# Optimization experiments

Measured on AMD Instinct MI355X. Metric: run time of the kernel, lower is better.

Reference implementation:

```python
import jax, jax.numpy as jnp
import numpy as np

B, N = 256, 256


def greedy_hard_perm(soft_perm):
    # soft_perm: (B, N, N). Sequential greedy masked-argmax assignment, vectorized over batch.
    Bn, Nn, _ = soft_perm.shape
    NEG = jnp.finfo(soft_perm.dtype).min
    b_idx = jnp.arange(Bn)

    def step(carry, _):
        scores, hard, row_mask, col_mask = carry
        # mask out already-assigned rows/cols (in-place masked_fill_ in torch -> carried scores)
        scores = jnp.where(row_mask[:, :, None], NEG, scores)
        scores = jnp.where(col_mask[:, None, :], NEG, scores)
        flat_idx = jnp.argmax(scores.reshape(Bn, -1), axis=1)  # (B,)
        r = flat_idx // Nn
        c = flat_idx % Nn
        hard = hard.at[b_idx, r, c].set(1.0)
        row_mask = row_mask.at[b_idx, r].set(True)
        col_mask = col_mask.at[b_idx, c].set(True)
        return (scores, hard, row_mask, col_mask), None

    init = (
        soft_perm,
        jnp.zeros_like(soft_perm),
        jnp.zeros((Bn, Nn), dtype=bool),
        jnp.zeros((Bn, Nn), dtype=bool),
    )
    (_, hard, _, _), _ = jax.lax.scan(step, init, None, length=Nn)
    return hard


def setup_inputs() -> dict:
    key = jax.random.key(0)
    logits = jax.random.normal(key, (B, N, N), dtype=jnp.float32)
    # realistic soft permutation: row-stochastic scores
    soft_perm = jax.nn.softmax(logits, axis=-1)
    return {"soft_perm": soft_perm}


def reference(soft_perm):
    # hard perm carries no gradient (built from constant 1.0 writes in torch)
    hard = greedy_hard_perm(jax.lax.stop_gradient(soft_perm))
    # straight-through estimator: forward = hard, backward = identity through soft
    return hard + soft_perm - jax.lax.stop_gradient(soft_perm)
```

## Files before the change

### kernel.cpp

```cpp
#include <hip/hip_runtime.h>
#include <math.h>

#define NEGINF (-INFINITY)
#define NEGINF_BITS ((int)0xFF800000)

typedef unsigned int u32;
typedef unsigned long long u64;

#define RST 64

__device__ __forceinline__ int rl_i(int x, int l) {
    return __builtin_amdgcn_readlane(x, l);
}
__device__ __forceinline__ float rl_f(float x, int l) {
    return __int_as_float(__builtin_amdgcn_readlane(__float_as_int(x), l));
}

template <int CTRL>
__device__ __forceinline__ float dppmax(float x) {
    int xi = __float_as_int(x);
    int yi = __builtin_amdgcn_update_dpp(xi, xi, CTRL, 0xf, 0xf, false);
    return fmaxf(x, __int_as_float(yi));
}

__device__ __forceinline__ float wave_max64(float x) {
    x = dppmax<0x111>(x);
    x = dppmax<0x112>(x);
    x = dppmax<0x114>(x);
    x = dppmax<0x118>(x);
    x = dppmax<0x142>(x);
    x = dppmax<0x143>(x);
    return rl_f(x, 63);
}

__device__ __forceinline__ void wave_argmax(float v, int idx, float& out_v, int& out_idx) {
    float mv = wave_max64(v);
    u64 mask = __ballot(v == mv);
    int ln = (int)__builtin_ctzll(mask);
    int bi = rl_i(idx, ln);
    u64 rest = mask & (mask - 1);
    if (rest) {
        while (rest) {
            int l2 = (int)__builtin_ctzll(rest); rest &= rest - 1;
            int b2 = rl_i(idx, l2);
            if (b2 < bi) bi = b2;
        }
    }
    out_v = mv; out_idx = bi;
}

__device__ __forceinline__ void wave_top2(float lv, int lf, float lv2, int lf2,
                                          float& nv, int& nc, float& nv2, int& nc2) {
    float av = lv, bv = lv2;
#define T2STAGE(CTRL) {                                                        \
        float a2 = __int_as_float(__builtin_amdgcn_update_dpp(                 \
            NEGINF_BITS, __float_as_int(av), CTRL, 0xf, 0xf, false));          \
        float b2 = __int_as_float(__builtin_amdgcn_update_dpp(                 \
            NEGINF_BITS, __float_as_int(bv), CTRL, 0xf, 0xf, false));          \
        float t = fminf(av, a2);                                               \
        av = fmaxf(av, a2);                                                    \
        bv = fmaxf(fmaxf(bv, b2), t); }
    T2STAGE(0x111) T2STAGE(0x112) T2STAGE(0x114) T2STAGE(0x118)
    T2STAGE(0x142) T2STAGE(0x143)
#undef T2STAGE
    nv = rl_f(av, 63);
    float sv = rl_f(bv, 63);

    u64 m1 = __ballot(lv == nv);
    int ln = (int)__builtin_ctzll(m1);
    nc = rl_i(lf, ln);

    nv2 = sv; nc2 = 300;
    if (sv > 0.f) {
        if (sv == nv) {
            float b2v = rl_f(lv2, ln);
            if (b2v == nv) {
                nc2 = rl_i(lf2, ln);
            } else {
                u64 rest = m1 & (m1 - 1);
                int l2 = (int)__builtin_ctzll(rest);
                nc2 = rl_i(lf, l2);
            }
        } else {
            u64 m2 = __ballot(lv == sv || lv2 == sv);
            int l2 = (int)__builtin_ctzll(m2);
            float tl = rl_f(lv, l2);
            nc2 = (tl == sv) ? rl_i(lf, l2) : rl_i(lf2, l2);
        }
    }
}

__global__ __launch_bounds__(64, 1) void greedy_perm_kernel(
        const float* __restrict__ soft, float* __restrict__ out) {
    __shared__ float smem[RST * 256];
    const int b = blockIdx.x;
    const int lane = threadIdx.x;
    const size_t base = (size_t)b << 16;
    const float* sc = soft + base;
    float* ob = out + base;

    float rv[4], spv[4];
    int   rc[4], spc[4];
#pragma unroll
    for (int j = 0; j < 4; ++j) { rv[j] = NEGINF; rc[j] = 0; spv[j] = NEGINF; spc[j] = 300; }

    const float4 zero4 = make_float4(0.f, 0.f, 0.f, 0.f);

    for (int k = 0; k < 64; k += 4) {
        float4 w[4][4];
#pragma unroll
        for (int j = 0; j < 4; ++j) {
            const float4* rp = (const float4*)(sc + (size_t)(j * 64 + lane) * 256);
#pragma unroll
            for (int kk = 0; kk < 4; ++kk) w[j][kk] = rp[k + kk];
        }
#pragma unroll
        for (int j = 0; j < 4; ++j) {
            float4* op = (float4*)(ob + (size_t)(j * 64 + lane) * 256);
#pragma unroll
            for (int kk = 0; kk < 4; ++kk) op[k + kk] = zero4;
        }
        {
            float* lp = &smem[lane << 8];
#pragma unroll
            for (int kk = 0; kk < 4; ++kk)
                *(float4*)&lp[((k + kk) ^ lane) << 2] = w[0][kk];
        }
#pragma unroll
        for (int j = 0; j < 4; ++j) {
#pragma unroll
            for (int kk = 0; kk < 4; ++kk) {
                const float4 ww = w[j][kk];
                const int bc = 4 * (k + kk);
                const float e[4] = {ww.x, ww.y, ww.z, ww.w};
#pragma unroll
                for (int q = 0; q < 4; ++q) {
                    const float x = e[q];
                    const int   cx = bc + q;
                    const bool g1 = x > rv[j];
                    const bool g2 = x > spv[j];
                    spv[j] = g1 ? rv[j] : (g2 ? x  : spv[j]);
                    spc[j] = g1 ? rc[j] : (g2 ? cx : spc[j]);
                    rv[j]  = g1 ? x  : rv[j];
                    rc[j]  = g1 ? cx : rc[j];
                }
            }
        }
    }

    __threadfence_block();

    u32 colmask = 0;

    for (int step = 0; step < 256; ++step) {
        float bv = rv[0];
        int   bf = (lane << 8) | (rc[0] & 255);
#pragma unroll
        for (int j = 1; j < 4; ++j) {
            if (rv[j] > bv) { bv = rv[j]; bf = (((j << 6) + lane) << 8) | (rc[j] & 255); }
        }
        float gv; int gf;
        wave_argmax(bv, bf, gv, gf);
        (void)gv;
        const int r  = gf >> 8;
        const int cc = gf & 255;

        if (lane == 0) ob[gf] = 1.0f;
        if (lane == (r & 63)) {
            const int rj = r >> 6;
#pragma unroll
            for (int j = 0; j < 4; ++j) if (j == rj) { rv[j] = NEGINF; rc[j] = 300; }
        }
        if (lane == (cc >> 2)) colmask |= 1u << (cc & 3);

#pragma unroll
        for (int j = 0; j < 4; ++j) if (spc[j] == cc) spc[j] = 300;

        bool dd[4]; bool anyd = false;
#pragma unroll
        for (int j = 0; j < 4; ++j) { dd[j] = (rc[j] == cc); anyd |= dd[j]; }
        if (__ballot(anyd)) {
#pragma unroll
            for (int j = 0; j < 4; ++j) {
                const bool need = dd[j] && (spc[j] == 300);
                if (dd[j] && !need) {
                    rv[j] = spv[j]; rc[j] = spc[j];
                    spv[j] = NEGINF; spc[j] = 300;
                }
                u64 m = __ballot(need);
                while (m) {
                    const int ln = (int)__builtin_ctzll(m); m &= m - 1;
                    const int row = (j << 6) + ln;
                    float4 w = (row < RST)
                        ? *(const float4*)&smem[(row << 8) | (((lane ^ ln) & 63) << 2)]
                        : *(const float4*)(sc + ((size_t)row << 8) + (lane << 2));
                    const float q0 = (colmask & 1u) ? NEGINF : w.x;
                    const float q1 = (colmask & 2u) ? NEGINF : w.y;
                    const float q2 = (colmask & 4u) ? NEGINF : w.z;
                    const float q3 = (colmask & 8u) ? NEGINF : w.w;
                    const int cb = lane << 2;
                    float lv = q0; int lf = cb;
                    float lv2 = NEGINF; int lf2 = cb;
                    {
                        bool g1 = q1 > lv, g2 = q1 > lv2;
                        lv2 = g1 ? lv : (g2 ? q1 : lv2); lf2 = g1 ? lf : (g2 ? cb + 1 : lf2);
                        lv  = g1 ? q1 : lv;              lf  = g1 ? cb + 1 : lf;
                        g1 = q2 > lv; g2 = q2 > lv2;
                        lv2 = g1 ? lv : (g2 ? q2 : lv2); lf2 = g1 ? lf : (g2 ? cb + 2 : lf2);
                        lv  = g1 ? q2 : lv;              lf  = g1 ? cb + 2 : lf;
                        g1 = q3 > lv; g2 = q3 > lv2;
                        lv2 = g1 ? lv : (g2 ? q3 : lv2); lf2 = g1 ? lf : (g2 ? cb + 3 : lf2);
                        lv  = g1 ? q3 : lv;              lf  = g1 ? cb + 3 : lf;
                    }
                    float nv, nv2; int nc, nc2;
                    wave_top2(lv, lf, lv2, lf2, nv, nc, nv2, nc2);
                    if (lane == ln) {
#pragma unroll
                        for (int jj = 0; jj < 4; ++jj) if (jj == j) {
                            rv[jj] = nv; rc[jj] = nc;
                            spv[jj] = nv2; spc[jj] = nc2;
                        }
                    }
                }
            }
        }
    }
}

extern "C" void kernel_launch(void* const* d_in, const int* in_sizes, int n_in,
                              void* d_out, int out_size, void* d_ws, size_t ws_size,
                              hipStream_t stream) {
    const float* soft = (const float*)d_in[0];
    float* out = (float*)d_out;
    const int n_batches = in_sizes[0] >> 16;

    greedy_perm_kernel<<<n_batches, 64, 0, stream>>>(soft, out);
}
```

Before: 300.9 us.

## Process two batches per wavefront with interleaved dual argmax reductions

Each 64-lane block now handles two batch matrices, interleaving their sequential greedy steps so the DPP max reductions, ballots and readlanes of the two independent chains can overlap and hide latency. The grid is halved to 128 blocks on a GPU with 256 CUs, so half the compute units sit idle. Shared-memory row caching per batch drops from 64 to 32 rows, so more refills must fall back to global loads. Register pressure roughly doubles.

```diff
diff --git a/kernel.cpp b/kernel.cpp
--- a/kernel.cpp
+++ b/kernel.cpp
@@ -7,7 +7,7 @@
 typedef unsigned int u32;
 typedef unsigned long long u64;
 
-#define RST 64
+#define RSTB 32
 
 __device__ __forceinline__ int rl_i(int x, int l) {
     return __builtin_amdgcn_readlane(x, l);
@@ -23,30 +23,50 @@
     return fmaxf(x, __int_as_float(yi));
 }
 
+template <int CTRL>
+__device__ __forceinline__ void dppmax2(float& a, float& b) {
+    int ai = __float_as_int(a), bi = __float_as_int(b);
+    int a2 = __builtin_amdgcn_update_dpp(ai, ai, CTRL, 0xf, 0xf, false);
+    int b2 = __builtin_amdgcn_update_dpp(bi, bi, CTRL, 0xf, 0xf, false);
+    a = fmaxf(a, __int_as_float(a2));
+    b = fmaxf(b, __int_as_float(b2));
+}
+
 __device__ __forceinline__ float wave_max64(float x) {
-    x = dppmax<0x111>(x);
-    x = dppmax<0x112>(x);
-    x = dppmax<0x114>(x);
-    x = dppmax<0x118>(x);
-    x = dppmax<0x142>(x);
-    x = dppmax<0x143>(x);
+    x = dppmax<0x111>(x); x = dppmax<0x112>(x); x = dppmax<0x114>(x);
+    x = dppmax<0x118>(x); x = dppmax<0x142>(x); x = dppmax<0x143>(x);
     return rl_f(x, 63);
 }
 
-__device__ __forceinline__ void wave_argmax(float v, int idx, float& out_v, int& out_idx) {
-    float mv = wave_max64(v);
-    u64 mask = __ballot(v == mv);
-    int ln = (int)__builtin_ctzll(mask);
-    int bi = rl_i(idx, ln);
-    u64 rest = mask & (mask - 1);
-    if (rest) {
-        while (rest) {
-            int l2 = (int)__builtin_ctzll(rest); rest &= rest - 1;
-            int b2 = rl_i(idx, l2);
-            if (b2 < bi) bi = b2;
-        }
-    }
-    out_v = mv; out_idx = bi;
+__device__ __forceinline__ void wave_argmax_dual(float vA, int idxA, float vB, int idxB,
+                                                 int& gfA, int& gfB) {
+    float xA = vA, xB = vB;
+    dppmax2<0x111>(xA, xB); dppmax2<0x112>(xA, xB); dppmax2<0x114>(xA, xB);
+    dppmax2<0x118>(xA, xB); dppmax2<0x142>(xA, xB); dppmax2<0x143>(xA, xB);
+    const float mvA = rl_f(xA, 63);
+    const float mvB = rl_f(xB, 63);
+    u64 mA = __ballot(vA == mvA);
+    u64 mB = __ballot(vB == mvB);
+    int lnA = (int)__builtin_ctzll(mA);
+    int lnB = (int)__builtin_ctzll(mB);
+    gfA = rl_i(idxA, lnA);
+    gfB = rl_i(idxB, lnB);
+    u64 rA = mA & (mA - 1);
+    u64 rB = mB & (mB - 1);
+    if (rA) {
+        while (rA) {
+            int l2 = (int)__builtin_ctzll(rA); rA &= rA - 1;
+            int f2 = rl_i(idxA, l2);
+            if (f2 < gfA) gfA = f2;
+        }
+    }
+    if (rB) {
+        while (rB) {
+            int l2 = (int)__builtin_ctzll(rB); rB &= rB - 1;
+            int f2 = rl_i(idxB, l2);
+            if (f2 < gfB) gfB = f2;
+        }
+    }
 }
 
 __device__ __forceinline__ void wave_top2(float lv, int lf, float lv2, int lf2,
@@ -91,58 +111,81 @@
 }
 
 __global__ __launch_bounds__(64, 1) void greedy_perm_kernel(
-        const float* __restrict__ soft, float* __restrict__ out) {
-    __shared__ float smem[RST * 256];
-    const int b = blockIdx.x;
+        const float* __restrict__ soft, float* __restrict__ out, int ntot) {
+    __shared__ float smem[2 * RSTB * 256];
     const int lane = threadIdx.x;
-    const size_t base = (size_t)b << 16;
-    const float* sc = soft + base;
-    float* ob = out + base;
-
-    float rv[4], spv[4];
-    int   rc[4], spc[4];
-#pragma unroll
-    for (int j = 0; j < 4; ++j) { rv[j] = NEGINF; rc[j] = 0; spv[j] = NEGINF; spc[j] = 300; }
+    const int b0 = blockIdx.x * 2;
+    const int b1 = (b0 + 1 < ntot) ? (b0 + 1) : b0;
+    const float* scA = soft + ((size_t)b0 << 16);
+    const float* scB = soft + ((size_t)b1 << 16);
+    float* obA = out + ((size_t)b0 << 16);
+    float* obB = out + ((size_t)b1 << 16);
+    float* smA = smem;
+    float* smB = smem + RSTB * 256;
+
+    float rvA[4], s1vA[4], rvB[4], s1vB[4];
+    int   rcA[4], s1cA[4], rcB[4], s1cB[4];
+#pragma unroll
+    for (int j = 0; j < 4; ++j) {
+        rvA[j] = NEGINF; rcA[j] = 0; s1vA[j] = NEGINF; s1cA[j] = 300;
+        rvB[j] = NEGINF; rcB[j] = 0; s1vB[j] = NEGINF; s1cB[j] = 300;
+    }
 
     const float4 zero4 = make_float4(0.f, 0.f, 0.f, 0.f);
 
     for (int k = 0; k < 64; k += 4) {
-        float4 w[4][4];
+        float4 wA[4][4], wB[4][4];
 #pragma unroll
         for (int j = 0; j < 4; ++j) {
-            const float4* rp = (const float4*)(sc + (size_t)(j * 64 + lane) * 256);
-#pragma unroll
-            for (int kk = 0; kk < 4; ++kk) w[j][kk] = rp[k + kk];
+            const float4* rpA = (const float4*)(scA + (size_t)(j * 64 + lane) * 256);
+            const float4* rpB = (const float4*)(scB + (size_t)(j * 64 + lane) * 256);
+#pragma unroll
+            for (int kk = 0; kk < 4; ++kk) { wA[j][kk] = rpA[k + kk]; wB[j][kk] = rpB[k + kk]; }
         }
 #pragma unroll
         for (int j = 0; j < 4; ++j) {
-            float4* op = (float4*)(ob + (size_t)(j * 64 + lane) * 256);
-#pragma unroll
-            for (int kk = 0; kk < 4; ++kk) op[k + kk] = zero4;
-        }
-        {
-            float* lp = &smem[lane << 8];
-#pragma unroll
-            for (int kk = 0; kk < 4; ++kk)
-                *(float4*)&lp[((k + kk) ^ lane) << 2] = w[0][kk];
+            float4* opA = (float4*)(obA + (size_t)(j * 64 + lane) * 256);
+            float4* opB = (float4*)(obB + (size_t)(j * 64 + lane) * 256);
+#pragma unroll
+            for (int kk = 0; kk < 4; ++kk) { opA[k + kk] = zero4; opB[k + kk] = zero4; }
+        }
+        if (lane < RSTB) {
+            float* lpA = &smA[lane << 8];
+            float* lpB = &smB[lane << 8];
+#pragma unroll
+            for (int kk = 0; kk < 4; ++kk) {
+                *(float4*)&lpA[((k + kk) ^ lane) << 2] = wA[0][kk];
+                *(float4*)&lpB[((k + kk) ^ lane) << 2] = wB[0][kk];
+            }
         }
 #pragma unroll
         for (int j = 0; j < 4; ++j) {
 #pragma unroll
             for (int kk = 0; kk < 4; ++kk) {
-                const float4 ww = w[j][kk];
                 const int bc = 4 * (k + kk);
-                const float e[4] = {ww.x, ww.y, ww.z, ww.w};
+                const float eA[4] = {wA[j][kk].x, wA[j][kk].y, wA[j][kk].z, wA[j][kk].w};
+                const float eB[4] = {wB[j][kk].x, wB[j][kk].y, wB[j][kk].z, wB[j][kk].w};
 #pragma unroll
                 for (int q = 0; q < 4; ++q) {
-                    const float x = e[q];
-                    const int   cx = bc + q;
-                    const bool g1 = x > rv[j];
-                    const bool g2 = x > spv[j];
-                    spv[j] = g1 ? rv[j] : (g2 ? x  : spv[j]);
-                    spc[j] = g1 ? rc[j] : (g2 ? cx : spc[j]);
-                    rv[j]  = g1 ? x  : rv[j];
-                    rc[j]  = g1 ? cx : rc[j];
+                    const int cx = bc + q;
+                    {
+                        const float x = eA[q];
+                        const bool g1 = x > rvA[j];
+                        const bool g2 = x > s1vA[j];
+                        s1vA[j] = g1 ? rvA[j] : (g2 ? x  : s1vA[j]);
+                        s1cA[j] = g1 ? rcA[j] : (g2 ? cx : s1cA[j]);
+                        rvA[j]  = g1 ? x  : rvA[j];
+                        rcA[j]  = g1 ? cx : rcA[j];
+                    }
+                    {
+                        const float x = eB[q];
+                        const bool g1 = x > rvB[j];
+                        const bool g2 = x > s1vB[j];
+                        s1vB[j] = g1 ? rvB[j] : (g2 ? x  : s1vB[j]);
+                        s1cB[j] = g1 ? rcB[j] : (g2 ? cx : s1cB[j]);
+                        rvB[j]  = g1 ? x  : rvB[j];
+                        rcB[j]  = g1 ? cx : rcB[j];
+                    }
                 }
             }
         }
@@ -150,54 +193,67 @@
 
     __threadfence_block();
 
-    u32 colmask = 0;
+    u32 cmA = 0, cmB = 0;
 
     for (int step = 0; step < 256; ++step) {
-        float bv = rv[0];
-        int   bf = (lane << 8) | (rc[0] & 255);
+        float bvA = rvA[0]; int bfA = (lane << 8) | (rcA[0] & 255);
+        float bvB = rvB[0]; int bfB = (lane << 8) | (rcB[0] & 255);
 #pragma unroll
         for (int j = 1; j < 4; ++j) {
-            if (rv[j] > bv) { bv = rv[j]; bf = (((j << 6) + lane) << 8) | (rc[j] & 255); }
-        }
-        float gv; int gf;
-        wave_argmax(bv, bf, gv, gf);
-        (void)gv;
-        const int r  = gf >> 8;
-        const int cc = gf & 255;
-
-        if (lane == 0) ob[gf] = 1.0f;
-        if (lane == (r & 63)) {
-            const int rj = r >> 6;
-#pragma unroll
-            for (int j = 0; j < 4; ++j) if (j == rj) { rv[j] = NEGINF; rc[j] = 300; }
-        }
-        if (lane == (cc >> 2)) colmask |= 1u << (cc & 3);
-
-#pragma unroll
-        for (int j = 0; j < 4; ++j) if (spc[j] == cc) spc[j] = 300;
-
-        bool dd[4]; bool anyd = false;
-#pragma unroll
-        for (int j = 0; j < 4; ++j) { dd[j] = (rc[j] == cc); anyd |= dd[j]; }
-        if (__ballot(anyd)) {
+            if (rvA[j] > bvA) { bvA = rvA[j]; bfA = (((j << 6) + lane) << 8) | (rcA[j] & 255); }
+            if (rvB[j] > bvB) { bvB = rvB[j]; bfB = (((j << 6) + lane) << 8) | (rcB[j] & 255); }
+        }
+
+        int gfA, gfB;
+        wave_argmax_dual(bvA, bfA, bvB, bfB, gfA, gfB);
+        const int rA = gfA >> 8, ccA = gfA & 255;
+        const int rB = gfB >> 8, ccB = gfB & 255;
+
+        if (lane == 0) { obA[gfA] = 1.0f; obB[gfB] = 1.0f; }
+
+        if (lane == (rA & 63)) {
+            const int rj = rA >> 6;
+#pragma unroll
+            for (int j = 0; j < 4; ++j) if (j == rj) { rvA[j] = NEGINF; rcA[j] = 300; }
+        }
+        if (lane == (ccA >> 2)) cmA |= 1u << (ccA & 3);
+#pragma unroll
+        for (int j = 0; j < 4; ++j) if (s1cA[j] == ccA) s1cA[j] = 300;
+        bool ddA[4]; bool anydA = false;
+#pragma unroll
+        for (int j = 0; j < 4; ++j) { ddA[j] = (rcA[j] == ccA); anydA |= ddA[j]; }
+
+        if (lane == (rB & 63)) {
+            const int rj = rB >> 6;
+#pragma unroll
+            for (int j = 0; j < 4; ++j) if (j == rj) { rvB[j] = NEGINF; rcB[j] = 300; }
+        }
+        if (lane == (ccB >> 2)) cmB |= 1u << (ccB & 3);
+#pragma unroll
+        for (int j = 0; j < 4; ++j) if (s1cB[j] == ccB) s1cB[j] = 300;
+        bool ddB[4]; bool anydB = false;
+#pragma unroll
+        for (int j = 0; j < 4; ++j) { ddB[j] = (rcB[j] == ccB); anydB |= ddB[j]; }
+
+        if (__ballot(anydA)) {
 #pragma unroll
             for (int j = 0; j < 4; ++j) {
-                const bool need = dd[j] && (spc[j] == 300);
-                if (dd[j] && !need) {
-                    rv[j] = spv[j]; rc[j] = spc[j];
-                    spv[j] = NEGINF; spc[j] = 300;
+                const bool need = ddA[j] && (s1cA[j] == 300);
+                if (ddA[j] && !need) {
+                    rvA[j] = s1vA[j]; rcA[j] = s1cA[j];
+                    s1vA[j] = NEGINF; s1cA[j] = 300;
                 }
                 u64 m = __ballot(need);
                 while (m) {
                     const int ln = (int)__builtin_ctzll(m); m &= m - 1;
                     const int row = (j << 6) + ln;
-                    float4 w = (row < RST)
-                        ? *(const float4*)&smem[(row << 8) | (((lane ^ ln) & 63) << 2)]
-                        : *(const float4*)(sc + ((size_t)row << 8) + (lane << 2));
-                    const float q0 = (colmask & 1u) ? NEGINF : w.x;
-                    const float q1 = (colmask & 2u) ? NEGINF : w.y;
-                    const float q2 = (colmask & 4u) ? NEGINF : w.z;
-                    const float q3 = (colmask & 8u) ? NEGINF : w.w;
+                    float4 w = (row < RSTB)
+                        ? *(const float4*)&smA[(row << 8) | (((lane ^ ln) & 63) << 2)]
+                        : *(const float4*)(scA + ((size_t)row << 8) + (lane << 2));
+                    const float q0 = (cmA & 1u) ? NEGINF : w.x;
+                    const float q1 = (cmA & 2u) ? NEGINF : w.y;
+                    const float q2 = (cmA & 4u) ? NEGINF : w.z;
+                    const float q3 = (cmA & 8u) ? NEGINF : w.w;
                     const int cb = lane << 2;
                     float lv = q0; int lf = cb;
                     float lv2 = NEGINF; int lf2 = cb;
@@ -217,8 +273,54 @@
                     if (lane == ln) {
 #pragma unroll
                         for (int jj = 0; jj < 4; ++jj) if (jj == j) {
-                            rv[jj] = nv; rc[jj] = nc;
-                            spv[jj] = nv2; spc[jj] = nc2;
+                            rvA[jj] = nv; rcA[jj] = nc;
+                            s1vA[jj] = nv2; s1cA[jj] = nc2;
+                        }
+                    }
+                }
+            }
+        }
+
+        if (__ballot(anydB)) {
+#pragma unroll
+            for (int j = 0; j < 4; ++j) {
+                const bool need = ddB[j] && (s1cB[j] == 300);
+                if (ddB[j] && !need) {
+                    rvB[j] = s1vB[j]; rcB[j] = s1cB[j];
+                    s1vB[j] = NEGINF; s1cB[j] = 300;
+                }
+                u64 m = __ballot(need);
+                while (m) {
+                    const int ln = (int)__builtin_ctzll(m); m &= m - 1;
+                    const int row = (j << 6) + ln;
+                    float4 w = (row < RSTB)
+                        ? *(const float4*)&smB[(row << 8) | (((lane ^ ln) & 63) << 2)]
+                        : *(const float4*)(scB + ((size_t)row << 8) + (lane << 2));
+                    const float q0 = (cmB & 1u) ? NEGINF : w.x;
+                    const float q1 = (cmB & 2u) ? NEGINF : w.y;
+                    const float q2 = (cmB & 4u) ? NEGINF : w.z;
+                    const float q3 = (cmB & 8u) ? NEGINF : w.w;
+                    const int cb = lane << 2;
+                    float lv = q0; int lf = cb;
+                    float lv2 = NEGINF; int lf2 = cb;
+                    {
+                        bool g1 = q1 > lv, g2 = q1 > lv2;
+                        lv2 = g1 ? lv : (g2 ? q1 : lv2); lf2 = g1 ? lf : (g2 ? cb + 1 : lf2);
+                        lv  = g1 ? q1 : lv;              lf  = g1 ? cb + 1 : lf;
+                        g1 = q2 > lv; g2 = q2 > lv2;
+                        lv2 = g1 ? lv : (g2 ? q2 : lv2); lf2 = g1 ? lf : (g2 ? cb + 2 : lf2);
+                        lv  = g1 ? q2 : lv;              lf  = g1 ? cb + 2 : lf;
+                        g1 = q3 > lv; g2 = q3 > lv2;
+                        lv2 = g1 ? lv : (g2 ? q3 : lv2); lf2 = g1 ? lf : (g2 ? cb + 3 : lf2);
+                        lv  = g1 ? q3 : lv;              lf  = g1 ? cb + 3 : lf;
+                    }
+                    float nv, nv2; int nc, nc2;
+                    wave_top2(lv, lf, lv2, lf2, nv, nc, nv2, nc2);
+                    if (lane == ln) {
+#pragma unroll
+                        for (int jj = 0; jj < 4; ++jj) if (jj == j) {
+                            rvB[jj] = nv; rcB[jj] = nc;
+                            s1vB[jj] = nv2; s1cB[jj] = nc2;
                         }
                     }
                 }
@@ -233,6 +335,7 @@
     const float* soft = (const float*)d_in[0];
     float* out = (float*)d_out;
     const int n_batches = in_sizes[0] >> 16;
-
-    greedy_perm_kernel<<<n_batches, 64, 0, stream>>>(soft, out);
-}
+    const int n_blocks = (n_batches + 1) >> 1;
+
+    greedy_perm_kernel<<<n_blocks, 64, 0, stream>>>(soft, out, n_batches);
+}
```

After: 498.0 us. 65.5% more time.
